# Kernel tuning notes

Hardware: AMD Instinct MI355X
Metric: run time of the kernel (lower is better)

Reference implementation:

```python
import jax, jax.numpy as jnp
import numpy as np

B, T, H, NSPK = 8, 1024, 1024, 2
LN_EPS = 1e-5


def setup_inputs() -> dict:
    key = jax.random.key(0)
    ks = jax.random.split(key, 12)
    s = 1.0 / np.sqrt(H)
    return {
        "x": jax.random.normal(ks[0], (B, T, H), jnp.float32),
        "qmask": jax.random.uniform(ks[1], (B, T, NSPK), jnp.float32),
        "dia_len": jax.random.randint(ks[2], (B,), T // 2, T + 1),
        "wp": 8,
        "wf": 8,
        "W_msg": jax.random.normal(ks[3], (H, H), jnp.float32) * s,
        "b_msg": jax.random.normal(ks[4], (H,), jnp.float32) * s,
        "W_self": jax.random.normal(ks[5], (H, H), jnp.float32) * s,
        "b_self": jax.random.normal(ks[6], (H,), jnp.float32) * s,
        "W_out": jax.random.normal(ks[7], (H, H), jnp.float32) * s,
        "b_out": jax.random.normal(ks[8], (H,), jnp.float32) * s,
        "gamma": jnp.ones((H,), jnp.float32),
        "beta": jnp.zeros((H,), jnp.float32),
    }


def reference(x, qmask, dia_len, wp, wf, W_msg, b_msg, W_self, b_self, W_out, b_out, gamma, beta):
    Bb, Tt, Hh = x.shape
    spk = jnp.argmax(qmask, axis=-1)                     # [B,T]
    pos = jnp.arange(Tt)
    offs = jnp.arange(-wp, wf + 1)                       # [W]
    idx = pos[:, None] + offs[None, :]                   # [T,W] window indices
    vlen = dia_len[:, None, None]                        # [B,1,1]
    valid = (idx[None] >= 0) & (idx[None] <= vlen - 1)   # [B,T,W]
    idxc = jnp.clip(idx, 0, Tt - 1)
    nb = jnp.take(x, idxc, axis=1)                       # [B,T,W,H]
    nb_spk = jnp.take(spk, idxc, axis=1)                 # [B,T,W]
    same = (nb_spk == spk[:, :, None]).astype(x.dtype)
    w = jnp.where(valid, 0.5 + 0.5 * same, 0.0)          # speaker weights, masked
    cnt = jnp.maximum(valid.sum(-1).astype(x.dtype), 1.0)  # window sizes [B,T]
    msg = jnp.einsum('btw,btwh->bth', w, nb) / cnt[..., None]
    h = x @ W_self + b_self + msg @ W_msg + b_msg        # per-node fusion
    node_valid = (pos[None, :] < dia_len[:, None])[..., None]
    out = jnp.where(node_valid, h, x)                    # nodes past dia_len keep x
    y = jax.nn.relu(out) @ W_out + b_out                 # dropout = identity (eval)
    z = x + y
    mean = z.mean(-1, keepdims=True)
    var = z.var(-1, keepdims=True)
    return gamma * (z - mean) / jnp.sqrt(var + LN_EPS) + beta
```

## Files before the change

kernel.cpp:

```cpp
#include <hip/hip_runtime.h>


typedef unsigned short u16;
typedef float floatx4 __attribute__((ext_vector_type(4)));
typedef short shortx8 __attribute__((ext_vector_type(8)));

#define T_ 1024
#define H_ 1024

__device__ __forceinline__ float bf2f(u16 v) {
    return __uint_as_float(((unsigned)v) << 16);
}
__device__ __forceinline__ u16 f2bf(float f) {
    unsigned u = __float_as_uint(f);
    return (u16)((u + 0x7fffu + ((u >> 16) & 1u)) >> 16);
}
__device__ __forceinline__ void async16(const void* g, void* l) {
    __builtin_amdgcn_global_load_lds(
        (__attribute__((address_space(1))) void*)g,
        (__attribute__((address_space(3))) void*)l, 16, 0, 0);
}

__global__ __launch_bounds__(256)
void transpose_pack(const float* __restrict__ Wself, const float* __restrict__ Wmsg,
                    const float* __restrict__ Wout,
                    u16* __restrict__ wt_cat, u16* __restrict__ wt_out)
{
    __shared__ float s[32][33];
    const int wid = blockIdx.z;
    const float* src = (wid == 0) ? Wself : ((wid == 1) ? Wmsg : Wout);
    const int n0 = blockIdx.x * 32, k0 = blockIdx.y * 32;
    const int tx = threadIdx.x & 31, ty = threadIdx.x >> 5;
#pragma unroll
    for (int i = 0; i < 4; ++i) {
        int k = k0 + ty + 8 * i;
        s[ty + 8 * i][tx] = src[(size_t)k * H_ + n0 + tx];
    }
    __syncthreads();
#pragma unroll
    for (int i = 0; i < 4; ++i) {
        int n = n0 + ty + 8 * i;
        u16 v = f2bf(s[tx][ty + 8 * i]);
        if (wid < 2) wt_cat[(size_t)n * 2048 + wid * 1024 + k0 + tx] = v;
        else         wt_out[(size_t)n * 1024 + k0 + tx] = v;
    }
}

__global__ __launch_bounds__(256)
void msg_pack(const float* __restrict__ x, const float* __restrict__ qmask,
              const int* __restrict__ dia_len, u16* __restrict__ xcat)
{
    __shared__ u16 sx[32][1024];
    const int tid = threadIdx.x;
    const int b = blockIdx.y;
    const int t0 = blockIdx.x * 16;
    const int dlen = dia_len[b];
    const int c4 = tid * 4;
    const float* xb = x + (size_t)b * T_ * H_;

    unsigned spkmask = 0;
#pragma unroll 4
    for (int r = 0; r < 32; ++r) {
        int row = t0 - 8 + r;
        row = row < 0 ? 0 : (row > T_ - 1 ? T_ - 1 : row);
        const float* q = qmask + ((size_t)b * T_ + row) * 2;
        spkmask |= (q[1] > q[0] ? 1u : 0u) << r;
        float4 v = *(const float4*)(xb + (size_t)row * H_ + c4);
        ushort4 u;
        u.x = f2bf(v.x); u.y = f2bf(v.y); u.z = f2bf(v.z); u.w = f2bf(v.w);
        *(ushort4*)&sx[r][c4] = u;
    }
    __syncthreads();

    for (int lt = 0; lt < 16; ++lt) {
        const int t = t0 + lt;
        const unsigned cs = (spkmask >> (lt + 8)) & 1u;
        float a0 = 0.f, a1 = 0.f, a2 = 0.f, a3 = 0.f;
        int cnt = 0;
#pragma unroll
        for (int o = 0; o < 17; ++o) {
            const int idx = t + o - 8;
            if (idx >= 0 && idx < dlen) {
                const float w = (((spkmask >> (lt + o)) & 1u) == cs) ? 1.0f : 0.5f;
                ++cnt;
                ushort4 u = *(const ushort4*)&sx[lt + o][c4];
                a0 += w * bf2f(u.x); a1 += w * bf2f(u.y);
                a2 += w * bf2f(u.z); a3 += w * bf2f(u.w);
            }
        }
        const float inv = 1.0f / (float)(cnt > 0 ? cnt : 1);
        ushort4 m;
        m.x = f2bf(a0 * inv); m.y = f2bf(a1 * inv);
        m.z = f2bf(a2 * inv); m.w = f2bf(a3 * inv);
        const size_t rowg = (size_t)b * T_ + t;
        *(ushort4*)&xcat[rowg * 2048 + 1024 + c4] = m;
        *(ushort4*)&xcat[rowg * 2048 + c4] = *(const ushort4*)&sx[lt + 8][c4];
    }
}

template <int K, int EPI>
__global__ __launch_bounds__(256)
void gemm_bt(const u16* __restrict__ A, const u16* __restrict__ Bt,
             const float* __restrict__ bias1, const float* __restrict__ bias2,
             const float* __restrict__ X, const int* __restrict__ dia_len,
             u16* __restrict__ Rout, float* __restrict__ Zout)
{
    constexpr int NT = K / 32;
    __shared__ u16 sA[4][128 * 32];
    __shared__ u16 sB[4][128 * 32];
    const int tid = threadIdx.x;
    const int bn = blockIdx.x * 128;
    const int bm = blockIdx.y * 128;
    const int wave = tid >> 6, lane = tid & 63;
    const int wr = wave >> 1, wc = wave & 1;
    const int lrow = lane & 15, lq = lane >> 4;

    const u16* gA0 = A + (size_t)(bm + (tid >> 2)) * K + (tid & 3) * 8;
    const u16* gA1 = gA0 + (size_t)64 * K;
    const u16* gB0 = Bt + (size_t)(bn + (tid >> 2)) * K + (tid & 3) * 8;
    const u16* gB1 = gB0 + (size_t)64 * K;
    const int lofs = wave * 512;

    auto stage = [&](int t) {
        const int s = t & 3;
        const int k0 = t * 32;
        u16* lA = &sA[s][0] + lofs;
        u16* lB = &sB[s][0] + lofs;
        async16(gA0 + k0, lA);
        async16(gA1 + k0, lA + 2048);
        async16(gB0 + k0, lB);
        async16(gB1 + k0, lB + 2048);
    };

    floatx4 acc[4][4];
#pragma unroll
    for (int i = 0; i < 4; ++i)
#pragma unroll
        for (int j = 0; j < 4; ++j)
            acc[i][j] = (floatx4){0.f, 0.f, 0.f, 0.f};

    const int pao = (wr * 64 + lrow) * 32 + lq * 8;
    const int pbo = (wc * 64 + lrow) * 32 + lq * 8;

    stage(0); stage(1); stage(2);

    for (int t = 0; t < NT; ++t) {
        if (t < NT - 2)       asm volatile("s_waitcnt vmcnt(8)" ::: "memory");
        else if (t == NT - 2) asm volatile("s_waitcnt vmcnt(4)" ::: "memory");
        else                  asm volatile("s_waitcnt vmcnt(0)" ::: "memory");
        __builtin_amdgcn_s_barrier();
        asm volatile("" ::: "memory");

        const u16* pa = &sA[t & 3][0] + pao;
        const u16* pb = &sB[t & 3][0] + pbo;
        shortx8 av[4], bv[4];
#pragma unroll
        for (int i = 0; i < 4; ++i) av[i] = *(const shortx8*)(pa + i * 512);
#pragma unroll
        for (int j = 0; j < 4; ++j) bv[j] = *(const shortx8*)(pb + j * 512);

        if (t + 3 < NT) stage(t + 3);

#pragma unroll
        for (int i = 0; i < 4; ++i)
#pragma unroll
            for (int j = 0; j < 4; ++j)
                acc[i][j] = __builtin_amdgcn_mfma_f32_16x16x32_bf16(
                    av[i], bv[j], acc[i][j], 0, 0, 0);
    }

    const int dl = (EPI == 1) ? dia_len[bm >> 10] : 0;
#pragma unroll
    for (int i = 0; i < 4; ++i) {
        const int row0 = bm + wr * 64 + i * 16 + lq * 4;
#pragma unroll
        for (int j = 0; j < 4; ++j) {
            const int col = bn + wc * 64 + j * 16 + lrow;
#pragma unroll
            for (int r = 0; r < 4; ++r) {
                const int row = row0 + r;
                const float v = acc[i][j][r];
                if (EPI == 1) {
                    const float h = v + bias1[col] + bias2[col];
                    float outv;
                    if ((row & (T_ - 1)) < dl) {
                        outv = h;
                    } else {
                        outv = X[(size_t)row * H_ + col];
                    }
                    Rout[(size_t)row * H_ + col] = f2bf(fmaxf(outv, 0.f));
                } else {
                    const float z = X[(size_t)row * H_ + col] + v + bias1[col];
                    Zout[(size_t)row * H_ + col] = z;
                }
            }
        }
    }
}

__global__ __launch_bounds__(256)
void ln_kernel(const float* __restrict__ Z, const float* __restrict__ gamma,
               const float* __restrict__ beta, float* __restrict__ out)
{
    const int row = blockIdx.x;
    const int tid = threadIdx.x;
    const size_t base = (size_t)row * H_ + tid * 4;
    float4 v = *(const float4*)(Z + base);
    float s = v.x + v.y + v.z + v.w;
    float q = v.x * v.x + v.y * v.y + v.z * v.z + v.w * v.w;
#pragma unroll
    for (int off = 32; off > 0; off >>= 1) {
        s += __shfl_down(s, off);
        q += __shfl_down(q, off);
    }
    __shared__ float ps[4], pq[4];
    const int wave = tid >> 6, lane = tid & 63;
    if (lane == 0) { ps[wave] = s; pq[wave] = q; }
    __syncthreads();
    const float S = ps[0] + ps[1] + ps[2] + ps[3];
    const float Q = pq[0] + pq[1] + pq[2] + pq[3];
    const float mean = S * (1.0f / 1024.0f);
    const float var = Q * (1.0f / 1024.0f) - mean * mean;
    const float inv = rsqrtf(var + 1e-5f);
    float4 g = *(const float4*)(gamma + tid * 4);
    float4 bt = *(const float4*)(beta + tid * 4);
    float4 o;
    o.x = g.x * (v.x - mean) * inv + bt.x;
    o.y = g.y * (v.y - mean) * inv + bt.y;
    o.z = g.z * (v.z - mean) * inv + bt.z;
    o.w = g.w * (v.w - mean) * inv + bt.w;
    *(float4*)(out + base) = o;
}

extern "C" void kernel_launch(void* const* d_in, const int* in_sizes, int n_in,
                              void* d_out, int out_size, void* d_ws, size_t ws_size,
                              hipStream_t stream)
{
    (void)in_sizes; (void)n_in; (void)out_size; (void)ws_size;
    const float* x       = (const float*)d_in[0];
    const float* qmask   = (const float*)d_in[1];
    const int*   dia_len = (const int*)d_in[2];
    const float* W_msg   = (const float*)d_in[5];
    const float* b_msg   = (const float*)d_in[6];
    const float* W_self  = (const float*)d_in[7];
    const float* b_self  = (const float*)d_in[8];
    const float* W_out   = (const float*)d_in[9];
    const float* b_out   = (const float*)d_in[10];
    const float* gamma   = (const float*)d_in[11];
    const float* beta    = (const float*)d_in[12];
    float* out = (float*)d_out;

    char* ws = (char*)d_ws;
    u16*   xcat   = (u16*)ws;
    u16*   rbuf   = (u16*)(ws + (size_t)(32u << 20));
    u16*   wt_cat = (u16*)(ws + (size_t)(48u << 20));
    u16*   wt_out = (u16*)(ws + (size_t)(52u << 20));
    float* zbuf   = (float*)ws;

    transpose_pack<<<dim3(32, 32, 3), 256, 0, stream>>>(W_self, W_msg, W_out, wt_cat, wt_out);
    msg_pack<<<dim3(64, 8), 256, 0, stream>>>(x, qmask, dia_len, xcat);
    gemm_bt<2048, 1><<<dim3(8, 64), 256, 0, stream>>>(xcat, wt_cat, b_self, b_msg,
                                                      x, dia_len, rbuf, nullptr);
    gemm_bt<1024, 2><<<dim3(8, 64), 256, 0, stream>>>(rbuf, wt_out, b_out, nullptr,
                                                      x, nullptr, nullptr, zbuf);
    ln_kernel<<<dim3(8192), 256, 0, stream>>>(zbuf, gamma, beta, out);
}
```

Measured before the change: 235.4 us.

## Restructure GEMM into 256x128 tiles with 512 threads, XOR-swizzled LDS and interleaved staging

The bf16 GEMM kernel now uses 512-thread blocks computing 256x128 output tiles with BK=64 and triple-buffered LDS. Staging is XOR-swizzled to avoid bank conflicts and split into chunks interleaved with MFMA phases, with s_setprio raised around the MFMA sections. A 1D grid with remapped block indices groups tiles for L2 locality. The aim is to raise MFMA utilisation and overlap global loads with compute, at the cost of more barriers and more LDS per block, which lowers occupancy.

```diff
diff --git a/kernel.cpp b/kernel.cpp
--- a/kernel.cpp
+++ b/kernel.cpp
@@ -19,6 +19,11 @@
     __builtin_amdgcn_global_load_lds(
         (__attribute__((address_space(1))) void*)g,
         (__attribute__((address_space(3))) void*)l, 16, 0, 0);
+}
+__device__ __forceinline__ void barrier_mem() {
+    asm volatile("" ::: "memory");
+    __builtin_amdgcn_s_barrier();
+    asm volatile("" ::: "memory");
 }
 
 __global__ __launch_bounds__(256)
@@ -99,37 +104,39 @@
 }
 
 template <int K, int EPI>
-__global__ __launch_bounds__(256)
+__global__ __launch_bounds__(512)
 void gemm_bt(const u16* __restrict__ A, const u16* __restrict__ Bt,
              const float* __restrict__ bias1, const float* __restrict__ bias2,
              const float* __restrict__ X, const int* __restrict__ dia_len,
              u16* __restrict__ Rout, float* __restrict__ Zout)
 {
-    constexpr int NT = K / 32;
-    __shared__ u16 sA[4][128 * 32];
-    __shared__ u16 sB[4][128 * 32];
+    constexpr int NT = K / 64;
+    __shared__ u16 sA[3][256 * 64];
+    __shared__ u16 sB[3][128 * 64];
     const int tid = threadIdx.x;
-    const int bn = blockIdx.x * 128;
-    const int bm = blockIdx.y * 128;
+
+    const int bid = blockIdx.x;
+    const int li = bid >> 3;
+    const int mt = (bid & 7) * 4 + (li >> 3);
+    const int nt = li & 7;
+    const int bm = mt * 256, bn = nt * 128;
+
     const int wave = tid >> 6, lane = tid & 63;
     const int wr = wave >> 1, wc = wave & 1;
     const int lrow = lane & 15, lq = lane >> 4;
 
-    const u16* gA0 = A + (size_t)(bm + (tid >> 2)) * K + (tid & 3) * 8;
-    const u16* gA1 = gA0 + (size_t)64 * K;
-    const u16* gB0 = Bt + (size_t)(bn + (tid >> 2)) * K + (tid & 3) * 8;
-    const u16* gB1 = gB0 + (size_t)64 * K;
-    const int lofs = wave * 512;
-
-    auto stage = [&](int t) {
-        const int s = t & 3;
-        const int k0 = t * 32;
-        u16* lA = &sA[s][0] + lofs;
-        u16* lB = &sB[s][0] + lofs;
-        async16(gA0 + k0, lA);
-        async16(gA1 + k0, lA + 2048);
-        async16(gB0 + k0, lB);
-        async16(gB1 + k0, lB + 2048);
+    const int srow = tid >> 3;
+    const int sl   = (tid & 7) ^ (srow & 7);
+    const u16* Asrc = A + (size_t)(bm + srow) * K + sl * 8;
+    const u16* Bsrc = Bt + (size_t)(bn + srow) * K + sl * 8;
+
+    auto stageA = [&](int t, int buf, int q) {
+        async16(Asrc + (size_t)q * 64 * K + t * 64,
+                &sA[buf][q * 4096 + tid * 8]);
+    };
+    auto stageB = [&](int t, int buf, int h) {
+        async16(Bsrc + (size_t)h * 64 * K + t * 64,
+                &sB[buf][h * 4096 + tid * 8]);
     };
 
     floatx4 acc[4][4];
@@ -139,34 +146,99 @@
         for (int j = 0; j < 4; ++j)
             acc[i][j] = (floatx4){0.f, 0.f, 0.f, 0.f};
 
-    const int pao = (wr * 64 + lrow) * 32 + lq * 8;
-    const int pbo = (wc * 64 + lrow) * 32 + lq * 8;
-
-    stage(0); stage(1); stage(2);
-
+    const int xk = lrow & 7;
+    const int paBase = (wr * 64 + lrow) * 64;
+    const int pbBase = (wc * 64 + lrow) * 64;
+    const int s0 = ((lq) ^ xk) * 8;
+    const int s1 = ((4 + lq) ^ xk) * 8;
+
+#pragma unroll
+    for (int q = 0; q < 4; ++q) stageA(0, 0, q);
+    stageB(0, 0, 0); stageB(0, 0, 1);
+#pragma unroll
+    for (int q = 0; q < 4; ++q) stageA(1, 1, q);
+    stageB(1, 1, 0); stageB(1, 1, 1);
+    asm volatile("s_waitcnt vmcnt(6)" ::: "memory");
+    barrier_mem();
+
+    int cur = 0, stg = 2;
     for (int t = 0; t < NT; ++t) {
-        if (t < NT - 2)       asm volatile("s_waitcnt vmcnt(8)" ::: "memory");
-        else if (t == NT - 2) asm volatile("s_waitcnt vmcnt(4)" ::: "memory");
-        else                  asm volatile("s_waitcnt vmcnt(0)" ::: "memory");
-        __builtin_amdgcn_s_barrier();
-        asm volatile("" ::: "memory");
-
-        const u16* pa = &sA[t & 3][0] + pao;
-        const u16* pb = &sB[t & 3][0] + pbo;
-        shortx8 av[4], bv[4];
-#pragma unroll
-        for (int i = 0; i < 4; ++i) av[i] = *(const shortx8*)(pa + i * 512);
-#pragma unroll
-        for (int j = 0; j < 4; ++j) bv[j] = *(const shortx8*)(pb + j * 512);
-
-        if (t + 3 < NT) stage(t + 3);
-
-#pragma unroll
-        for (int i = 0; i < 4; ++i)
+        const u16* curA = &sA[cur][0];
+        const u16* curB = &sB[cur][0];
+        const bool more = (t + 2 < NT);
+        shortx8 a0[4], b0[4], a1[4], b1[4];
+
+#pragma unroll
+        for (int j = 0; j < 4; ++j)
+            b0[j] = *(const shortx8*)(curB + pbBase + j * 1024 + s0);
+#pragma unroll
+        for (int i = 0; i < 2; ++i)
+            a0[i] = *(const shortx8*)(curA + paBase + i * 1024 + s0);
+        if (more) { stageA(t + 2, stg, 0); stageA(t + 2, stg, 1); }
+        barrier_mem();
+        __builtin_amdgcn_s_setprio(1);
+#pragma unroll
+        for (int i = 0; i < 2; ++i)
 #pragma unroll
             for (int j = 0; j < 4; ++j)
                 acc[i][j] = __builtin_amdgcn_mfma_f32_16x16x32_bf16(
-                    av[i], bv[j], acc[i][j], 0, 0, 0);
+                    a0[i], b0[j], acc[i][j], 0, 0, 0);
+        __builtin_amdgcn_s_setprio(0);
+        barrier_mem();
+
+#pragma unroll
+        for (int i = 2; i < 4; ++i)
+            a0[i] = *(const shortx8*)(curA + paBase + i * 1024 + s0);
+        if (more) { stageA(t + 2, stg, 2); stageA(t + 2, stg, 3); }
+        barrier_mem();
+        __builtin_amdgcn_s_setprio(1);
+#pragma unroll
+        for (int i = 2; i < 4; ++i)
+#pragma unroll
+            for (int j = 0; j < 4; ++j)
+                acc[i][j] = __builtin_amdgcn_mfma_f32_16x16x32_bf16(
+                    a0[i], b0[j], acc[i][j], 0, 0, 0);
+        __builtin_amdgcn_s_setprio(0);
+        barrier_mem();
+
+#pragma unroll
+        for (int j = 0; j < 4; ++j)
+            b1[j] = *(const shortx8*)(curB + pbBase + j * 1024 + s1);
+#pragma unroll
+        for (int i = 0; i < 2; ++i)
+            a1[i] = *(const shortx8*)(curA + paBase + i * 1024 + s1);
+        if (more) { stageB(t + 2, stg, 0); stageB(t + 2, stg, 1); }
+        barrier_mem();
+        __builtin_amdgcn_s_setprio(1);
+#pragma unroll
+        for (int i = 0; i < 2; ++i)
+#pragma unroll
+            for (int j = 0; j < 4; ++j)
+                acc[i][j] = __builtin_amdgcn_mfma_f32_16x16x32_bf16(
+                    a1[i], b1[j], acc[i][j], 0, 0, 0);
+        __builtin_amdgcn_s_setprio(0);
+        barrier_mem();
+
+#pragma unroll
+        for (int i = 2; i < 4; ++i)
+            a1[i] = *(const shortx8*)(curA + paBase + i * 1024 + s1);
+        barrier_mem();
+        __builtin_amdgcn_s_setprio(1);
+#pragma unroll
+        for (int i = 2; i < 4; ++i)
+#pragma unroll
+            for (int j = 0; j < 4; ++j)
+                acc[i][j] = __builtin_amdgcn_mfma_f32_16x16x32_bf16(
+                    a1[i], b1[j], acc[i][j], 0, 0, 0);
+        __builtin_amdgcn_s_setprio(0);
+
+        if (t < NT - 1) {
+            if (more) asm volatile("s_waitcnt vmcnt(6)" ::: "memory");
+            else      asm volatile("s_waitcnt vmcnt(0)" ::: "memory");
+            barrier_mem();
+        }
+        cur = (cur == 2) ? 0 : cur + 1;
+        stg = (stg == 2) ? 0 : stg + 1;
     }
 
     const int dl = (EPI == 1) ? dia_len[bm >> 10] : 0;
@@ -259,9 +331,9 @@
 
     transpose_pack<<<dim3(32, 32, 3), 256, 0, stream>>>(W_self, W_msg, W_out, wt_cat, wt_out);
     msg_pack<<<dim3(64, 8), 256, 0, stream>>>(x, qmask, dia_len, xcat);
-    gemm_bt<2048, 1><<<dim3(8, 64), 256, 0, stream>>>(xcat, wt_cat, b_self, b_msg,
-                                                      x, dia_len, rbuf, nullptr);
-    gemm_bt<1024, 2><<<dim3(8, 64), 256, 0, stream>>>(rbuf, wt_out, b_out, nullptr,
-                                                      x, nullptr, nullptr, zbuf);
+    gemm_bt<2048, 1><<<dim3(256), 512, 0, stream>>>(xcat, wt_cat, b_self, b_msg,
+                                                    x, dia_len, rbuf, nullptr);
+    gemm_bt<1024, 2><<<dim3(256), 512, 0, stream>>>(rbuf, wt_out, b_out, nullptr,
+                                                    x, nullptr, nullptr, zbuf);
     ln_kernel<<<dim3(8192), 256, 0, stream>>>(zbuf, gamma, beta, out);
 }
```

Measured after the change: 240.9 us. 2.4% more time.
